# Kernel tuning notes

Hardware: AMD Instinct MI355X
Metric: run time of the kernel (lower is better)

Reference implementation:

```python
import jax, jax.numpy as jnp
import numpy as np

# dims
B, D_IN, HID, G, K = 64, 5000, 1000, 512, 8
N_LABELS, GROUP_SIZE, M = 262144, 512, 32
C = K * GROUP_SIZE  # candidates per sample after topk group expansion


def setup_inputs() -> dict:
    key = jax.random.key(0)
    ks = jax.random.split(key, 8)
    x = jax.random.normal(ks[0], (B, D_IN), jnp.float32)
    candidates = jax.random.randint(ks[1], (B, M), 0, N_LABELS, dtype=jnp.int32)
    labels = (jax.random.uniform(ks[2], (B, M)) < 0.2).astype(jnp.float32)
    group_labels = (jax.random.uniform(ks[3], (B, G)) < 0.05).astype(jnp.float32)
    W1 = jax.random.normal(ks[4], (HID, D_IN), jnp.float32) * 0.02
    b1 = jnp.zeros((HID,), jnp.float32)
    W2 = jax.random.normal(ks[5], (G, HID), jnp.float32) * 0.02
    b2 = jnp.zeros((G,), jnp.float32)
    emb = jax.random.normal(ks[6], (N_LABELS, G), jnp.float32) * 0.02
    # equal-size contiguous groups (makes the torch pad-to-max a no-op)
    group_y = jnp.arange(N_LABELS, dtype=jnp.int32).reshape(G, GROUP_SIZE)
    return dict(x=x, candidates=candidates, labels=labels, group_labels=group_labels,
                W1=W1, b1=b1, W2=W2, b2=b2, emb=emb, group_y=group_y)


def _bce_with_logits(z, t):
    # mean over all elements of log(1+e^z) - z*t (stable)
    return jnp.mean(jnp.logaddexp(0.0, z) - z * t)


def reference(x, candidates, labels, group_labels, W1, b1, W2, b2, emb, group_y):
    # router MLP: Linear -> ReLU -> Linear -> sigmoid
    h = jax.nn.relu(x @ W1.T + b1)                 # [B, HID]
    y = jax.nn.sigmoid(h @ W2.T + b2)              # [B, G]
    # topk group select on detached scores
    _, idx = jax.lax.top_k(jax.lax.stop_gradient(y), K)   # [B, K]
    cand = group_y[idx].reshape(B, C)              # [B, C] gathered candidate label ids
    # build per-candidate binary targets: candidate is positive iff it appears
    # among the masked ground-truth candidates of that sample
    tgt = jnp.where(labels > 0.5, candidates, -1)  # [B, M]
    new_labels = (cand[:, :, None] == tgt[:, None, :]).any(-1).astype(jnp.float32)  # [B, C]
    # gathered embedding bmm scoring
    ew = emb[cand]                                 # [B, C, G]
    logits = jnp.einsum('bcg,bg->bc', ew, y)       # [B, C]
    loss = _bce_with_logits(logits, new_labels) + _bce_with_logits(y, group_labels)
    return logits, loss
```

## Files before the change

### kernel.cpp

```cpp
#include <hip/hip_runtime.h>
#include <math.h>

static constexpr int BB  = 64;
static constexpr int DIN = 5000;
static constexpr int NHID = 1000;
static constexpr int NG  = 512;
static constexpr int NK  = 8;
static constexpr int NM  = 32;
static constexpr int GS  = 512;
static constexpr int NC  = NK * GS;
static constexpr int NPAIR = BB * NK;

static constexpr int S1 = 16, CHD1 = 320, IT1 = 16, IP1 = 1024;
static constexpr int S2 = 16, CHD2 = 64,  IT2 = 8,  IP2 = 512;

__global__ __launch_bounds__(256) void gemm64(
    const float* __restrict__ A, int lda,
    const float* __restrict__ Bm, int ldb, int Ireal,
    float* __restrict__ part, int Ipad, int Itiles, int D, int CHD)
{
  __shared__ __align__(16) float xT[32][64];
  __shared__ __align__(16) float wT[32][64];
  const int tid = threadIdx.x;
  const int itile = blockIdx.x % Itiles;
  const int s = blockIdx.x / Itiles;
  const int d_beg = s * CHD;
  const int d_end = min(D, d_beg + CHD);
  const int tx = tid & 15;
  const int ty = tid >> 4;
  float acc[4][4] = {};

  for (int d0 = d_beg; d0 < d_end; d0 += 32) {
#pragma unroll
    for (int q = 0; q < 2; q++) {
      int lin = q * 256 + tid;
      int r = lin >> 3;
      int c4 = (lin & 7) << 2;
      int d = d0 + c4;
      const float* pr = A + (size_t)r * lda;
      float4 v = make_float4(0.f, 0.f, 0.f, 0.f);
      if (d + 4 <= d_end) v = *(const float4*)(pr + d);
      else {
        if (d + 0 < d_end) v.x = pr[d + 0];
        if (d + 1 < d_end) v.y = pr[d + 1];
        if (d + 2 < d_end) v.z = pr[d + 2];
        if (d + 3 < d_end) v.w = pr[d + 3];
      }
      xT[c4 + 0][r] = v.x; xT[c4 + 1][r] = v.y;
      xT[c4 + 2][r] = v.z; xT[c4 + 3][r] = v.w;
    }
#pragma unroll
    for (int q = 0; q < 2; q++) {
      int lin = q * 256 + tid;
      int r = lin >> 3;
      int c4 = (lin & 7) << 2;
      int ib = itile * 64 + r;
      int d = d0 + c4;
      float4 v = make_float4(0.f, 0.f, 0.f, 0.f);
      if (ib < Ireal) {
        const float* pr = Bm + (size_t)ib * ldb;
        if (d + 4 <= d_end) v = *(const float4*)(pr + d);
        else {
          if (d + 0 < d_end) v.x = pr[d + 0];
          if (d + 1 < d_end) v.y = pr[d + 1];
          if (d + 2 < d_end) v.z = pr[d + 2];
          if (d + 3 < d_end) v.w = pr[d + 3];
        }
      }
      wT[c4 + 0][r] = v.x; wT[c4 + 1][r] = v.y;
      wT[c4 + 2][r] = v.z; wT[c4 + 3][r] = v.w;
    }
    __syncthreads();
    const int nn = min(32, d_end - d0);
    if (nn == 32) {
#pragma unroll
      for (int dd = 0; dd < 32; dd++) {
        float4 xv = *(const float4*)&xT[dd][tx << 2];
        float4 wv = *(const float4*)&wT[dd][ty << 2];
        float xr[4] = {xv.x, xv.y, xv.z, xv.w};
        float wr[4] = {wv.x, wv.y, wv.z, wv.w};
#pragma unroll
        for (int a = 0; a < 4; a++)
#pragma unroll
          for (int c = 0; c < 4; c++)
            acc[a][c] = fmaf(xr[a], wr[c], acc[a][c]);
      }
    } else {
      for (int dd = 0; dd < nn; dd++) {
        float4 xv = *(const float4*)&xT[dd][tx << 2];
        float4 wv = *(const float4*)&wT[dd][ty << 2];
        float xr[4] = {xv.x, xv.y, xv.z, xv.w};
        float wr[4] = {wv.x, wv.y, wv.z, wv.w};
#pragma unroll
        for (int a = 0; a < 4; a++)
#pragma unroll
          for (int c = 0; c < 4; c++)
            acc[a][c] = fmaf(xr[a], wr[c], acc[a][c]);
      }
    }
    __syncthreads();
  }

  const int b0 = tx << 2;
  const int i0 = itile * 64 + (ty << 2);
#pragma unroll
  for (int a = 0; a < 4; a++) {
    float4 vv = make_float4(acc[a][0], acc[a][1], acc[a][2], acc[a][3]);
    *(float4*)&part[((size_t)s * BB + (b0 + a)) * Ipad + i0] = vv;
  }
}

__global__ void reduce_act(const float* __restrict__ part, int S, int Ipad, int Ireal,
                           const float* __restrict__ bias, float* __restrict__ out,
                           int ostride, int mode)
{
  int lin = blockIdx.x * blockDim.x + threadIdx.x;
  int n = BB * Ireal;
  if (lin >= n) return;
  int b = lin / Ireal;
  int i = lin - b * Ireal;
  float sum = bias[i];
  for (int s = 0; s < S; s++) sum += part[((size_t)s * BB + b) * Ipad + i];
  if (mode == 0) sum = fmaxf(sum, 0.f);
  else           sum = 1.f / (1.f + expf(-sum));
  out[(size_t)b * ostride + i] = sum;
}

__global__ __launch_bounds__(64) void topk_loss2(
    const float* __restrict__ y, const float* __restrict__ gl,
    int* __restrict__ idxo, float* __restrict__ acc)
{
  const int b = blockIdx.x;
  const int lane = threadIdx.x;
  float v[8];
  float l2 = 0.f;
#pragma unroll
  for (int j = 0; j < 8; j++) {
    int pos = j * 64 + lane;
    float z = y[b * NG + pos];
    v[j] = z;
    float t = gl[b * NG + pos];
    l2 += fmaxf(z, 0.f) + log1pf(expf(-fabsf(z))) - z * t;
  }
  for (int k = 0; k < 8; k++) {
    float bv = -INFINITY;
    int bi = 0x7fffffff;
#pragma unroll
    for (int j = 0; j < 8; j++) {
      int pos = j * 64 + lane;
      if (v[j] > bv) { bv = v[j]; bi = pos; }
    }
#pragma unroll
    for (int off = 32; off >= 1; off >>= 1) {
      float ov = __shfl_xor(bv, off, 64);
      int   oi = __shfl_xor(bi, off, 64);
      if (ov > bv || (ov == bv && oi < bi)) { bv = ov; bi = oi; }
    }
    if (lane == 0) idxo[b * NK + k] = bi;
    if (lane == (bi & 63)) {
      int jj = bi >> 6;
#pragma unroll
      for (int j = 0; j < 8; j++) if (j == jj) v[j] = -INFINITY;
    }
  }
#pragma unroll
  for (int off = 32; off >= 1; off >>= 1) l2 += __shfl_xor(l2, off, 64);
  if (lane == 0) atomicAdd(acc + 1, l2);
}

__global__ __launch_bounds__(512) void sort_pairs(
    const int* __restrict__ idxb, int* __restrict__ order)
{
  __shared__ int gs[NPAIR];
  const int i = threadIdx.x;
  gs[i] = idxb[i];
  __syncthreads();
  const int g = gs[i];
  int pos = 0;
  for (int j = 0; j < NPAIR; j++) {
    int gj = gs[j];
    pos += (gj < g) || (gj == g && j < i);
  }
  order[pos] = i;
}

__global__ __launch_bounds__(512) void score3(
    const float* __restrict__ emb, const float* __restrict__ y,
    const int* __restrict__ order, const int* __restrict__ idxb,
    const int* __restrict__ cands, const float* __restrict__ labels,
    const int* __restrict__ group_y, float* __restrict__ out,
    float* __restrict__ acc)
{
  const int L = (blockIdx.x & 7) * 128 + (blockIdx.x >> 3);
  const int pair = order[L >> 1];
  const int half = L & 1;
  const int b = pair >> 3;
  const int g = idxb[pair];
  __shared__ __align__(16) float yl[NG];
  __shared__ int cid[256];
  __shared__ int tgt[NM];
  __shared__ float red[8];
  const int tid = threadIdx.x;
  yl[tid] = y[b * NG + tid];
  if (tid < 256) cid[tid] = group_y[g * GS + half * 256 + tid];
  if (tid >= 256 && tid < 256 + NM) {
    int m = tid - 256;
    tgt[m] = labels[b * NM + m] > 0.5f ? cands[b * NM + m] : -1;
  }
  __syncthreads();

  const int l = tid & 15;
  const int grp = tid >> 4;
  const float4* yl4 = (const float4*)yl;
  float lossp = 0.f;

  for (int it = 0; it < 8; it++) {
    int rloc = it * 32 + grp;
    int row = half * 256 + rloc;
    int r = cid[rloc];
    const float4* ep = (const float4*)(emb + (size_t)r * NG);
    float sum = 0.f;
#pragma unroll
    for (int seg = 0; seg < 8; seg++) {
      float4 e  = ep[seg * 16 + l];
      float4 yv = yl4[seg * 16 + l];
      sum = fmaf(e.x, yv.x, sum);
      sum = fmaf(e.y, yv.y, sum);
      sum = fmaf(e.z, yv.z, sum);
      sum = fmaf(e.w, yv.w, sum);
    }
    sum += __shfl_xor(sum, 1, 64);
    sum += __shfl_xor(sum, 2, 64);
    sum += __shfl_xor(sum, 4, 64);
    sum += __shfl_xor(sum, 8, 64);
    if (l == 0) {
      out[(size_t)pair * GS + row] = sum;
      float nl = 0.f;
#pragma unroll
      for (int m = 0; m < NM; m++) if (r == tgt[m]) nl = 1.f;
      lossp += fmaxf(sum, 0.f) + log1pf(expf(-fabsf(sum))) - sum * nl;
    }
  }
#pragma unroll
  for (int off = 32; off >= 1; off >>= 1) lossp += __shfl_xor(lossp, off, 64);
  const int wid = tid >> 6;
  if ((tid & 63) == 0) red[wid] = lossp;
  __syncthreads();
  if (tid == 0) {
    float t = 0.f;
#pragma unroll
    for (int w = 0; w < 8; w++) t += red[w];
    atomicAdd(acc, t);
  }
}

__global__ void finalize_loss(const float* __restrict__ acc, float* __restrict__ out)
{
  out[(size_t)BB * NC] = acc[0] * (1.f / (float)(BB * NC)) +
                         acc[1] * (1.f / (float)(BB * NG));
}

extern "C" void kernel_launch(void* const* d_in, const int* in_sizes, int n_in,
                              void* d_out, int out_size, void* d_ws, size_t ws_size,
                              hipStream_t stream)
{
  const float* x      = (const float*)d_in[0];
  const int*   cands  = (const int*)  d_in[1];
  const float* labels = (const float*)d_in[2];
  const float* glab   = (const float*)d_in[3];
  const float* W1     = (const float*)d_in[4];
  const float* b1     = (const float*)d_in[5];
  const float* W2     = (const float*)d_in[6];
  const float* b2     = (const float*)d_in[7];
  const float* emb    = (const float*)d_in[8];
  const int*   gy     = (const int*)  d_in[9];
  float* out = (float*)d_out;

  float* ws   = (float*)d_ws;
  float* acc  = ws;
  float* y    = ws + 16;
  int*   idxb = (int*)(y + BB * NG);
  float* h    = (float*)(idxb + NPAIR);
  float* p1   = h + (size_t)BB * IP1;
  float* p2   = p1 + (size_t)S1 * BB * IP1;
  int*   order = (int*)(p2 + (size_t)S2 * BB * IP2);

  hipMemsetAsync(acc, 0, 2 * sizeof(float), stream);

  gemm64<<<IT1 * S1, 256, 0, stream>>>(x, DIN, W1, DIN, NHID, p1, IP1, IT1, DIN, CHD1);
  reduce_act<<<(BB * NHID + 255) / 256, 256, 0, stream>>>(p1, S1, IP1, NHID, b1, h, IP1, 0);

  gemm64<<<IT2 * S2, 256, 0, stream>>>(h, IP1, W2, NHID, NG, p2, IP2, IT2, NHID, CHD2);
  reduce_act<<<(BB * NG + 255) / 256, 256, 0, stream>>>(p2, S2, IP2, NG, b2, y, NG, 1);

  topk_loss2<<<BB, 64, 0, stream>>>(y, glab, idxb, acc);

  sort_pairs<<<1, NPAIR, 0, stream>>>(idxb, order);

  score3<<<2 * NPAIR, 512, 0, stream>>>(emb, y, order, idxb, cands, labels, gy, out, acc);

  finalize_loss<<<1, 1, 0, stream>>>(acc, out);
}
```

Before: 125.0 us.

## Score two sorted pairs per block, reusing embedding rows when groups match

The scoring kernel now gives each block two adjacent pairs from the group-sorted order, each block covering a quarter of the group's 512 candidates. When both pairs selected the same group, every embedding row is loaded once and dotted against both samples' router outputs, which roughly halves gathered embedding traffic for duplicate groups. When the groups differ it falls back to two separate passes. It adds shared memory and registers for the second sample and a divergent branch per block.

After: 142.3 us. 13.9% more time.

```diff
diff --git a/kernel.cpp b/kernel.cpp
--- a/kernel.cpp
+++ b/kernel.cpp
@@ -184,7 +184,7 @@
   order[pos] = i;
 }
 
-__global__ __launch_bounds__(512) void score3(
+__global__ __launch_bounds__(512) void score_duo(
     const float* __restrict__ emb, const float* __restrict__ y,
     const int* __restrict__ order, const int* __restrict__ idxb,
     const int* __restrict__ cands, const float* __restrict__ labels,
@@ -192,55 +192,109 @@
     float* __restrict__ acc)
 {
   const int L = (blockIdx.x & 7) * 128 + (blockIdx.x >> 3);
-  const int pair = order[L >> 1];
-  const int half = L & 1;
-  const int b = pair >> 3;
-  const int g = idxb[pair];
-  __shared__ __align__(16) float yl[NG];
-  __shared__ int cid[256];
-  __shared__ int tgt[NM];
+  const int d = L >> 2;
+  const int q = L & 3;
+  const int pa = order[2 * d], pb = order[2 * d + 1];
+  const int ba = pa >> 3, bb = pb >> 3;
+  const int ga = idxb[pa], gb = idxb[pb];
+
+  __shared__ __align__(16) float ya[NG];
+  __shared__ __align__(16) float yb[NG];
+  __shared__ int cida[128];
+  __shared__ int cidb[128];
+  __shared__ int tga[NM];
+  __shared__ int tgb[NM];
   __shared__ float red[8];
   const int tid = threadIdx.x;
-  yl[tid] = y[b * NG + tid];
-  if (tid < 256) cid[tid] = group_y[g * GS + half * 256 + tid];
-  if (tid >= 256 && tid < 256 + NM) {
+  ya[tid] = y[ba * NG + tid];
+  yb[tid] = y[bb * NG + tid];
+  if (tid < 128) cida[tid] = group_y[ga * GS + q * 128 + tid];
+  else if (tid < 256) cidb[tid - 128] = group_y[gb * GS + q * 128 + (tid - 128)];
+  else if (tid < 256 + NM) {
     int m = tid - 256;
-    tgt[m] = labels[b * NM + m] > 0.5f ? cands[b * NM + m] : -1;
+    tga[m] = labels[ba * NM + m] > 0.5f ? cands[ba * NM + m] : -1;
+  } else if (tid < 256 + 2 * NM) {
+    int m = tid - 256 - NM;
+    tgb[m] = labels[bb * NM + m] > 0.5f ? cands[bb * NM + m] : -1;
   }
   __syncthreads();
 
-  const int l = tid & 15;
-  const int grp = tid >> 4;
-  const float4* yl4 = (const float4*)yl;
+  const int l = tid & 15, lg = tid >> 4;
+  const float4* ya4 = (const float4*)ya;
+  const float4* yb4 = (const float4*)yb;
   float lossp = 0.f;
 
-  for (int it = 0; it < 8; it++) {
-    int rloc = it * 32 + grp;
-    int row = half * 256 + rloc;
-    int r = cid[rloc];
-    const float4* ep = (const float4*)(emb + (size_t)r * NG);
-    float sum = 0.f;
-#pragma unroll
-    for (int seg = 0; seg < 8; seg++) {
-      float4 e  = ep[seg * 16 + l];
-      float4 yv = yl4[seg * 16 + l];
-      sum = fmaf(e.x, yv.x, sum);
-      sum = fmaf(e.y, yv.y, sum);
-      sum = fmaf(e.z, yv.z, sum);
-      sum = fmaf(e.w, yv.w, sum);
-    }
-    sum += __shfl_xor(sum, 1, 64);
-    sum += __shfl_xor(sum, 2, 64);
-    sum += __shfl_xor(sum, 4, 64);
-    sum += __shfl_xor(sum, 8, 64);
-    if (l == 0) {
-      out[(size_t)pair * GS + row] = sum;
-      float nl = 0.f;
-#pragma unroll
-      for (int m = 0; m < NM; m++) if (r == tgt[m]) nl = 1.f;
-      lossp += fmaxf(sum, 0.f) + log1pf(expf(-fabsf(sum))) - sum * nl;
-    }
-  }
+  if (ga == gb) {
+    for (int it = 0; it < 4; it++) {
+      const int rloc = it * 32 + lg;
+      const int row = q * 128 + rloc;
+      const int rid = cida[rloc];
+      const float4* ep = (const float4*)(emb + (size_t)rid * NG);
+      float4 e[8];
+#pragma unroll
+      for (int seg = 0; seg < 8; seg++) e[seg] = ep[seg * 16 + l];
+      float sa = 0.f, sb = 0.f;
+#pragma unroll
+      for (int seg = 0; seg < 8; seg++) {
+        float4 av = ya4[seg * 16 + l];
+        float4 bv = yb4[seg * 16 + l];
+        sa = fmaf(e[seg].x, av.x, sa); sb = fmaf(e[seg].x, bv.x, sb);
+        sa = fmaf(e[seg].y, av.y, sa); sb = fmaf(e[seg].y, bv.y, sb);
+        sa = fmaf(e[seg].z, av.z, sa); sb = fmaf(e[seg].z, bv.z, sb);
+        sa = fmaf(e[seg].w, av.w, sa); sb = fmaf(e[seg].w, bv.w, sb);
+      }
+#pragma unroll
+      for (int off = 8; off >= 1; off >>= 1) {
+        sa += __shfl_xor(sa, off, 64);
+        sb += __shfl_xor(sb, off, 64);
+      }
+      if (l == 0) {
+        out[(size_t)pa * GS + row] = sa;
+        out[(size_t)pb * GS + row] = sb;
+        float nla = 0.f, nlb = 0.f;
+#pragma unroll
+        for (int m = 0; m < NM; m++) {
+          if (rid == tga[m]) nla = 1.f;
+          if (rid == tgb[m]) nlb = 1.f;
+        }
+        lossp += fmaxf(sa, 0.f) + log1pf(expf(-fabsf(sa))) - sa * nla;
+        lossp += fmaxf(sb, 0.f) + log1pf(expf(-fabsf(sb))) - sb * nlb;
+      }
+    }
+  } else {
+    for (int side = 0; side < 2; side++) {
+      const int pp = side ? pb : pa;
+      const int* cc = side ? cidb : cida;
+      const float4* yy = side ? yb4 : ya4;
+      const int* tt = side ? tgb : tga;
+      for (int it = 0; it < 4; it++) {
+        const int rloc = it * 32 + lg;
+        const int row = q * 128 + rloc;
+        const int rid = cc[rloc];
+        const float4* ep = (const float4*)(emb + (size_t)rid * NG);
+        float s = 0.f;
+#pragma unroll
+        for (int seg = 0; seg < 8; seg++) {
+          float4 e = ep[seg * 16 + l];
+          float4 yv = yy[seg * 16 + l];
+          s = fmaf(e.x, yv.x, s);
+          s = fmaf(e.y, yv.y, s);
+          s = fmaf(e.z, yv.z, s);
+          s = fmaf(e.w, yv.w, s);
+        }
+#pragma unroll
+        for (int off = 8; off >= 1; off >>= 1) s += __shfl_xor(s, off, 64);
+        if (l == 0) {
+          out[(size_t)pp * GS + row] = s;
+          float nl = 0.f;
+#pragma unroll
+          for (int m = 0; m < NM; m++) if (rid == tt[m]) nl = 1.f;
+          lossp += fmaxf(s, 0.f) + log1pf(expf(-fabsf(s))) - s * nl;
+        }
+      }
+    }
+  }
+
 #pragma unroll
   for (int off = 32; off >= 1; off >>= 1) lossp += __shfl_xor(lossp, off, 64);
   const int wid = tid >> 6;
@@ -297,7 +351,7 @@
 
   sort_pairs<<<1, NPAIR, 0, stream>>>(idxb, order);
 
-  score3<<<2 * NPAIR, 512, 0, stream>>>(emb, y, order, idxb, cands, labels, gy, out, acc);
+  score_duo<<<2 * NPAIR, 512, 0, stream>>>(emb, y, order, idxb, cands, labels, gy, out, acc);
 
   finalize_loss<<<1, 1, 0, stream>>>(acc, out);
 }
```

## Convert selected group embeddings to bf16 once, then score from bf16 copy

Applied to the files above, without the earlier changes.

Sort now also marks the first occurrence of each selected group. A new kernel converts that group's 512 embedding rows from fp32 to bf16 into a large workspace buffer, once per unique group. A new scoring kernel then reads the bf16 rows, halving the bytes loaded per candidate. The path only runs when the workspace is large enough, adds a full extra read and write pass over the unique groups, and lowers the precision of the logits.

After: 214.2 us. 71.4% more time.

```diff
diff --git a/kernel.cpp b/kernel.cpp
--- a/kernel.cpp
+++ b/kernel.cpp
@@ -13,6 +13,12 @@
 
 static constexpr int S1 = 16, CHD1 = 320, IT1 = 16, IP1 = 1024;
 static constexpr int S2 = 16, CHD2 = 64,  IT2 = 8,  IP2 = 512;
+
+__device__ inline unsigned short f2bf(float f) {
+  unsigned int u = __float_as_uint(f);
+  unsigned int r = (u + 0x7fffu + ((u >> 16) & 1u)) >> 16;
+  return (unsigned short)r;
+}
 
 __global__ __launch_bounds__(256) void gemm64(
     const float* __restrict__ A, int lda,
@@ -169,23 +175,53 @@
 }
 
 __global__ __launch_bounds__(512) void sort_pairs(
-    const int* __restrict__ idxb, int* __restrict__ order)
+    const int* __restrict__ idxb, int* __restrict__ order,
+    int* __restrict__ heads)
 {
   __shared__ int gs[NPAIR];
   const int i = threadIdx.x;
   gs[i] = idxb[i];
   __syncthreads();
   const int g = gs[i];
-  int pos = 0;
+  int pos = 0, first = 0;
   for (int j = 0; j < NPAIR; j++) {
     int gj = gs[j];
-    pos += (gj < g) || (gj == g && j < i);
+    int lt = (gj < g);
+    pos += lt | ((gj == g) & (j < i));
+    first += lt;
   }
   order[pos] = i;
-}
-
-__global__ __launch_bounds__(512) void score3(
-    const float* __restrict__ emb, const float* __restrict__ y,
+  heads[pos] = (pos == first) ? 1 : 0;
+}
+
+__global__ __launch_bounds__(256) void conv_bf16(
+    const float* __restrict__ emb, const int* __restrict__ heads,
+    const int* __restrict__ order, const int* __restrict__ idxb,
+    unsigned short* __restrict__ ebf)
+{
+  const int rank = blockIdx.x >> 1;
+  if (!heads[rank]) return;
+  const int half = blockIdx.x & 1;
+  const int g = idxb[order[rank]];
+  const size_t base = (size_t)g * GS * NG + (size_t)half * (GS / 2) * NG;
+  const float4* s4 = (const float4*)(emb + base);
+  uint4* d4 = (uint4*)(ebf + base);
+  const int tid = threadIdx.x;
+  for (int i = 0; i < 64; i++) {
+    int idx = i * 256 + tid;
+    float4 a = s4[2 * idx];
+    float4 b = s4[2 * idx + 1];
+    uint4 o;
+    o.x = (unsigned int)f2bf(a.x) | ((unsigned int)f2bf(a.y) << 16);
+    o.y = (unsigned int)f2bf(a.z) | ((unsigned int)f2bf(a.w) << 16);
+    o.z = (unsigned int)f2bf(b.x) | ((unsigned int)f2bf(b.y) << 16);
+    o.w = (unsigned int)f2bf(b.z) | ((unsigned int)f2bf(b.w) << 16);
+    d4[idx] = o;
+  }
+}
+
+__global__ __launch_bounds__(512) void score3bf(
+    const unsigned short* __restrict__ ebf, const float* __restrict__ y,
     const int* __restrict__ order, const int* __restrict__ idxb,
     const int* __restrict__ cands, const float* __restrict__ labels,
     const int* __restrict__ group_y, float* __restrict__ out,
@@ -203,7 +239,84 @@
   const int tid = threadIdx.x;
   yl[tid] = y[b * NG + tid];
   if (tid < 256) cid[tid] = group_y[g * GS + half * 256 + tid];
-  if (tid >= 256 && tid < 256 + NM) {
+  else if (tid >= 256 && tid < 256 + NM) {
+    int m = tid - 256;
+    tgt[m] = labels[b * NM + m] > 0.5f ? cands[b * NM + m] : -1;
+  }
+  __syncthreads();
+
+  const int l = tid & 15;
+  const int grp = tid >> 4;
+  const float4* yl4 = (const float4*)yl;
+  float lossp = 0.f;
+
+  for (int it = 0; it < 8; it++) {
+    int rloc = it * 32 + grp;
+    int row = half * 256 + rloc;
+    int r = cid[rloc];
+    const uint4* ep = (const uint4*)(ebf + (size_t)r * NG);
+    uint4 e[4];
+#pragma unroll
+    for (int seg = 0; seg < 4; seg++) e[seg] = ep[seg * 16 + l];
+    float sum = 0.f;
+#pragma unroll
+    for (int seg = 0; seg < 4; seg++) {
+      float4 y0 = yl4[(seg * 16 + l) * 2];
+      float4 y1 = yl4[(seg * 16 + l) * 2 + 1];
+      sum = fmaf(__uint_as_float(e[seg].x << 16), y0.x, sum);
+      sum = fmaf(__uint_as_float(e[seg].x & 0xffff0000u), y0.y, sum);
+      sum = fmaf(__uint_as_float(e[seg].y << 16), y0.z, sum);
+      sum = fmaf(__uint_as_float(e[seg].y & 0xffff0000u), y0.w, sum);
+      sum = fmaf(__uint_as_float(e[seg].z << 16), y1.x, sum);
+      sum = fmaf(__uint_as_float(e[seg].z & 0xffff0000u), y1.y, sum);
+      sum = fmaf(__uint_as_float(e[seg].w << 16), y1.z, sum);
+      sum = fmaf(__uint_as_float(e[seg].w & 0xffff0000u), y1.w, sum);
+    }
+    sum += __shfl_xor(sum, 1, 64);
+    sum += __shfl_xor(sum, 2, 64);
+    sum += __shfl_xor(sum, 4, 64);
+    sum += __shfl_xor(sum, 8, 64);
+    if (l == 0) {
+      out[(size_t)pair * GS + row] = sum;
+      float nl = 0.f;
+#pragma unroll
+      for (int m = 0; m < NM; m++) if (r == tgt[m]) nl = 1.f;
+      lossp += fmaxf(sum, 0.f) + log1pf(expf(-fabsf(sum))) - sum * nl;
+    }
+  }
+#pragma unroll
+  for (int off = 32; off >= 1; off >>= 1) lossp += __shfl_xor(lossp, off, 64);
+  const int wid = tid >> 6;
+  if ((tid & 63) == 0) red[wid] = lossp;
+  __syncthreads();
+  if (tid == 0) {
+    float t = 0.f;
+#pragma unroll
+    for (int w = 0; w < 8; w++) t += red[w];
+    atomicAdd(acc, t);
+  }
+}
+
+__global__ __launch_bounds__(512) void score3(
+    const float* __restrict__ emb, const float* __restrict__ y,
+    const int* __restrict__ order, const int* __restrict__ idxb,
+    const int* __restrict__ cands, const float* __restrict__ labels,
+    const int* __restrict__ group_y, float* __restrict__ out,
+    float* __restrict__ acc)
+{
+  const int L = (blockIdx.x & 7) * 128 + (blockIdx.x >> 3);
+  const int pair = order[L >> 1];
+  const int half = L & 1;
+  const int b = pair >> 3;
+  const int g = idxb[pair];
+  __shared__ __align__(16) float yl[NG];
+  __shared__ int cid[256];
+  __shared__ int tgt[NM];
+  __shared__ float red[8];
+  const int tid = threadIdx.x;
+  yl[tid] = y[b * NG + tid];
+  if (tid < 256) cid[tid] = group_y[g * GS + half * 256 + tid];
+  else if (tid >= 256 && tid < 256 + NM) {
     int m = tid - 256;
     tgt[m] = labels[b * NM + m] > 0.5f ? cands[b * NM + m] : -1;
   }
@@ -284,6 +397,10 @@
   float* p1   = h + (size_t)BB * IP1;
   float* p2   = p1 + (size_t)S1 * BB * IP1;
   int*   order = (int*)(p2 + (size_t)S2 * BB * IP2);
+  int*   heads = order + NPAIR;
+  unsigned short* ebf = (unsigned short*)((char*)d_ws + ((size_t)8 << 20));
+  const bool use_bf = ws_size >= (((size_t)8 << 20) +
+                                  (size_t)262144 * NG * sizeof(unsigned short));
 
   hipMemsetAsync(acc, 0, 2 * sizeof(float), stream);
 
@@ -295,9 +412,14 @@
 
   topk_loss2<<<BB, 64, 0, stream>>>(y, glab, idxb, acc);
 
-  sort_pairs<<<1, NPAIR, 0, stream>>>(idxb, order);
-
-  score3<<<2 * NPAIR, 512, 0, stream>>>(emb, y, order, idxb, cands, labels, gy, out, acc);
+  sort_pairs<<<1, NPAIR, 0, stream>>>(idxb, order, heads);
+
+  if (use_bf) {
+    conv_bf16<<<2 * NPAIR, 256, 0, stream>>>(emb, heads, order, idxb, ebf);
+    score3bf<<<2 * NPAIR, 512, 0, stream>>>(ebf, y, order, idxb, cands, labels, gy, out, acc);
+  } else {
+    score3<<<2 * NPAIR, 512, 0, stream>>>(emb, y, order, idxb, cands, labels, gy, out, acc);
+  }
 
   finalize_loss<<<1, 1, 0, stream>>>(acc, out);
 }
```
